# Optimization experiments

Hardware: AMD Instinct MI355X
Metric: run time of the kernel (lower is better)

## Reference

```python
import jax, jax.numpy as jnp
import numpy as np

KN = 2048       # 12*N spatio-temporal tokens
B = 4           # batch
D_MODEL = 512
N_HEADS = 8
HEAD_DIM = D_MODEL // N_HEADS
FACTOR = 5
U_PART = min(FACTOR * int(np.ceil(np.log(KN))), KN)  # sample_k == n_top == 40


def setup_inputs() -> dict:
    rng = jax.random.key(0)
    ks = jax.random.split(rng, 12)
    d = D_MODEL
    wscale = 1.0 / np.sqrt(d)  # xavier-ish init scale
    return {
        "query": jax.random.normal(ks[0], (KN, B, d), jnp.float32),
        "key": jax.random.normal(ks[1], (KN, B, d), jnp.float32),
        "value": jax.random.normal(ks[2], (KN, B, d), jnp.float32),
        "index_sample": jax.random.randint(ks[3], (KN, U_PART), 0, KN),
        "Wq": jax.random.normal(ks[4], (d, d), jnp.float32) * wscale,
        "bq": jnp.zeros((d,), jnp.float32),
        "Wk": jax.random.normal(ks[5], (d, d), jnp.float32) * wscale,
        "bk": jnp.zeros((d,), jnp.float32),
        "Wv": jax.random.normal(ks[6], (d, d), jnp.float32) * wscale,
        "bv": jnp.zeros((d,), jnp.float32),
        "Wo": jax.random.normal(ks[7], (d, d), jnp.float32) * wscale,
        "bo": jnp.zeros((d,), jnp.float32),
    }


def reference(query, key, value, index_sample, Wq, bq, Wk, bk, Wv, bv, Wo, bo):
    kN, Bb, d = query.shape
    H, E = N_HEADS, HEAD_DIM
    scaling = E ** -0.5

    # projections (torch Linear: x @ W.T + b); q is scaled before reshaping
    q = (query @ Wq.T + bq) * scaling
    k = key @ Wk.T + bk
    v = value @ Wv.T + bv

    # [kN, B, d] -> [B, H, kN, E]
    def to_bhne(x):
        return x.reshape(kN, Bb, H, E).transpose(1, 2, 0, 3)

    Q, K, V = to_bhne(q), to_bhne(k), to_bhne(v)

    # ProbSparse: sample U_PART keys per query row (shared index table)
    K_samp = K[:, :, index_sample, :]                       # [B,H,kN,S,E]
    QK_samp = jnp.einsum('bhne,bhnse->bhns', Q, K_samp)      # [B,H,kN,S]
    # sparsity measure M = max - mean(over full kN, as in source)
    M = QK_samp.max(axis=-1) - QK_samp.sum(axis=-1) / kN     # [B,H,kN]
    _, M_top = jax.lax.top_k(M, U_PART)                      # [B,H,S]

    # reduced queries attend over ALL keys
    Q_red = jnp.take_along_axis(Q, M_top[..., None], axis=2)  # [B,H,S,E]
    scores = jnp.einsum('bhse,bhne->bhsn', Q_red, K)          # [B,H,S,kN]
    attn = jax.nn.softmax(scores, axis=-1)
    upd = jnp.einsum('bhsn,bhne->bhse', attn, V)              # [B,H,S,E]

    # initial context = mean(V) broadcast; scatter-update the top rows
    ctx = jnp.broadcast_to(V.mean(axis=2, keepdims=True), V.shape)  # [B,H,kN,E]
    bi = jnp.arange(Bb)[:, None, None]
    hi = jnp.arange(H)[None, :, None]
    ctx = ctx.at[bi, hi, M_top].set(upd)

    out = ctx.transpose(0, 2, 1, 3).reshape(Bb, kN, d) @ Wo.T + bo  # [B,kN,d]
    return out
```

## Files before the change

### kernel.cpp

```cpp
#include <hip/hip_runtime.h>
#include <hip/hip_bf16.h>

#define KN 2048
#define BB 4
#define DM 512
#define NH 8
#define HE 64
#define UP 40
#define NBH 32
#define NROWS 8192
#define MiB(x) ((size_t)(x) << 20)

typedef __attribute__((ext_vector_type(8))) short short8;
typedef __attribute__((ext_vector_type(4))) float f32x4;

__device__ __forceinline__ ushort f2bf(float x) {
  unsigned u = __float_as_uint(x);
  unsigned r = (u + 0x7FFFu + ((u >> 16) & 1u)) >> 16;
  return (ushort)r;
}
__device__ __forceinline__ float bf2f(ushort h) {
  return __uint_as_float((unsigned)h << 16);
}

__global__ __launch_bounds__(256) void wsplit3_kernel(
    const float* __restrict__ W0, const float* __restrict__ W1,
    const float* __restrict__ W2, ushort* __restrict__ Wh,
    ushort* __restrict__ Wl) {
  const int which = blockIdx.x >> 9;
  const float* W = (which == 0) ? W0 : (which == 1) ? W1 : W2;
  size_t base = (size_t)which * 262144;
  int i = ((blockIdx.x & 511) * 256 + threadIdx.x) * 2;
  float2 v = *(const float2*)(W + i);
  ushort h0 = f2bf(v.x), h1 = f2bf(v.y);
  ushort l0 = f2bf(v.x - bf2f(h0)), l1 = f2bf(v.y - bf2f(h1));
  *(ushort2*)(Wh + base + i) = make_ushort2(h0, h1);
  *(ushort2*)(Wl + base + i) = make_ushort2(l0, l1);
}

#define APAD 40
__global__ __launch_bounds__(256) void gemm3_mfma(
    const float* __restrict__ A0, const float* __restrict__ A1,
    const float* __restrict__ A2,
    const ushort* __restrict__ Wh3, const ushort* __restrict__ Wl3,
    const float* __restrict__ bq, const float* __restrict__ bk,
    const float* __restrict__ bv, float* __restrict__ QKV) {
  __shared__ ushort AsH[2][64 * APAD];
  __shared__ ushort AsL[2][64 * APAD];

  const int which = blockIdx.x >> 8;
  const int local = blockIdx.x & 255;
  const int xcd = local & 7;
  const int idx = local >> 3;
  const int ot = idx >> 4;
  const int mt = xcd * 16 + (idx & 15);
  const int m0 = mt * 64, o0 = ot * 256;

  const float* A = (which == 0) ? A0 : (which == 1) ? A1 : A2;
  const ushort* Wh = Wh3 + (size_t)which * 262144;
  const ushort* Wl = Wl3 + (size_t)which * 262144;
  const float* bias = (which == 0) ? bq : (which == 1) ? bk : bv;
  float* C = QKV + (size_t)which * 8192 * 512;
  const float scale = (which == 0) ? 0.125f : 1.0f;

  const int tid = threadIdx.x;
  const int w = tid >> 6, lane = tid & 63;
  const int fr = lane & 15;
  const int kc = lane >> 4;

  f32x4 acc[4][4];
#pragma unroll
  for (int i = 0; i < 4; ++i)
#pragma unroll
    for (int j = 0; j < 4; ++j)
#pragma unroll
      for (int r = 0; r < 4; ++r) acc[i][j][r] = 0.f;

  const int srow0 = tid >> 3, sq0 = tid & 7;
  const int srow1 = (tid + 256) >> 3, sq1 = (tid + 256) & 7;

#define STAGE_A(BUF, K0)                                                    \
  do {                                                                      \
    float4 v0 = *(const float4*)(A + (size_t)(m0 + srow0) * 512 + (K0) + sq0 * 4); \
    float4 v1 = *(const float4*)(A + (size_t)(m0 + srow1) * 512 + (K0) + sq1 * 4); \
    ushort h0 = f2bf(v0.x), h1 = f2bf(v0.y), h2 = f2bf(v0.z), h3 = f2bf(v0.w); \
    *(ushort4*)(&AsH[BUF][srow0 * APAD + sq0 * 4]) = make_ushort4(h0, h1, h2, h3); \
    *(ushort4*)(&AsL[BUF][srow0 * APAD + sq0 * 4]) = make_ushort4(           \
        f2bf(v0.x - bf2f(h0)), f2bf(v0.y - bf2f(h1)),                        \
        f2bf(v0.z - bf2f(h2)), f2bf(v0.w - bf2f(h3)));                       \
    ushort g0 = f2bf(v1.x), g1 = f2bf(v1.y), g2 = f2bf(v1.z), g3 = f2bf(v1.w); \
    *(ushort4*)(&AsH[BUF][srow1 * APAD + sq1 * 4]) = make_ushort4(g0, g1, g2, g3); \
    *(ushort4*)(&AsL[BUF][srow1 * APAD + sq1 * 4]) = make_ushort4(           \
        f2bf(v1.x - bf2f(g0)), f2bf(v1.y - bf2f(g1)),                        \
        f2bf(v1.z - bf2f(g2)), f2bf(v1.w - bf2f(g3)));                       \
  } while (0)

  STAGE_A(0, 0);

#pragma unroll
  for (int it = 0; it < 16; ++it) {
    const int cur = it & 1;
    const int k0 = it * 32;
    __syncthreads();
    if (it + 1 < 16) STAGE_A(!cur ? 1 : 0, k0 + 32);

    short8 ah[4], al[4], bh[4], bl[4];
#pragma unroll
    for (int i = 0; i < 4; ++i) {
      int off = (i * 16 + fr) * APAD + kc * 8;
      ah[i] = *(const short8*)(&AsH[cur][off]);
      al[i] = *(const short8*)(&AsL[cur][off]);
    }
#pragma unroll
    for (int j = 0; j < 4; ++j) {
      size_t off = (size_t)(o0 + w * 64 + j * 16 + fr) * 512 + k0 + kc * 8;
      bh[j] = *(const short8*)(Wh + off);
      bl[j] = *(const short8*)(Wl + off);
    }
#pragma unroll
    for (int i = 0; i < 4; ++i)
#pragma unroll
      for (int j = 0; j < 4; ++j) {
        acc[i][j] = __builtin_amdgcn_mfma_f32_16x16x32_bf16(
            ah[i], bh[j], acc[i][j], 0, 0, 0);
        acc[i][j] = __builtin_amdgcn_mfma_f32_16x16x32_bf16(
            ah[i], bl[j], acc[i][j], 0, 0, 0);
        acc[i][j] = __builtin_amdgcn_mfma_f32_16x16x32_bf16(
            al[i], bh[j], acc[i][j], 0, 0, 0);
      }
  }

#pragma unroll
  for (int i = 0; i < 4; ++i)
#pragma unroll
    for (int j = 0; j < 4; ++j)
#pragma unroll
      for (int r = 0; r < 4; ++r) {
        int m = m0 + i * 16 + (lane >> 4) * 4 + r;
        int o = o0 + w * 64 + j * 16 + fr;
        C[(size_t)m * 512 + o] = (acc[i][j][r] + bias[o]) * scale;
      }
}

__global__ __launch_bounds__(256) void transposeK_kernel(
    const float* __restrict__ K, float* __restrict__ Kt) {
  const int bh = blockIdx.x & 31;
  const int nt = blockIdx.x >> 5;
  const int b = bh >> 3, h = bh & 7;
  const int n0 = nt * 128;
  const int tid = threadIdx.x;
  __shared__ float T[128][65];

#pragma unroll
  for (int i = 0; i < 8; ++i) {
    int flat = tid + i * 256;
    int r = flat >> 4;
    int c4 = flat & 15;
    float4 v = *(const float4*)(K + (((size_t)(n0 + r) * 4 + b) * 8 + h) * 64 + c4 * 4);
    T[r][c4 * 4 + 0] = v.x; T[r][c4 * 4 + 1] = v.y;
    T[r][c4 * 4 + 2] = v.z; T[r][c4 * 4 + 3] = v.w;
  }
  __syncthreads();

  const int nl = tid & 127;
  const int eg = tid >> 7;
#pragma unroll
  for (int e = eg * 32; e < eg * 32 + 32; ++e)
    Kt[((size_t)bh * 64 + e) * 2048 + n0 + nl] = T[nl][e];
}

__global__ __launch_bounds__(256) void mscore_kernel(
    const float* __restrict__ Q, const float* __restrict__ K,
    const int* __restrict__ idx, float* __restrict__ Mout) {
  const int bh = blockIdx.x & 31;
  const int c  = blockIdx.x >> 5;
  const int wv = threadIdx.x >> 6;
  const int lane = threadIdx.x & 63;
  const int n = c * 4 + wv;
  const int b = bh >> 3, h = bh & 7;
  const int g = lane >> 4;
  const int e16 = lane & 15;

  const float4 qv = *(const float4*)(Q + (((size_t)n * 4 + b) * 8 + h) * 64 + e16 * 4);

  float mx = -INFINITY, sm = 0.f;
#pragma unroll
  for (int it = 0; it < 10; ++it) {
    const int s = it * 4 + g;
    const int kn = idx[n * UP + s];
    const float4 kv = *(const float4*)(K + (((size_t)kn * 4 + b) * 8 + h) * 64 + e16 * 4);
    float d = qv.x * kv.x + qv.y * kv.y + qv.z * kv.z + qv.w * kv.w;
    d += __shfl_xor(d, 1);
    d += __shfl_xor(d, 2);
    d += __shfl_xor(d, 4);
    d += __shfl_xor(d, 8);
    mx = fmaxf(mx, d);
    sm += d;
  }
  mx = fmaxf(mx, __shfl_xor(mx, 16));
  mx = fmaxf(mx, __shfl_xor(mx, 32));
  sm += __shfl_xor(sm, 16);
  sm += __shfl_xor(sm, 32);
  if (lane == 0) Mout[(size_t)bh * 2048 + n] = mx - sm * (1.0f / (float)KN);
}

__global__ __launch_bounds__(256) void topk_kernel(
    const float* __restrict__ M, int* __restrict__ Mtop) {
  const int bh = blockIdx.x;
  __shared__ unsigned keys[2048];
  __shared__ int hist[256];
  __shared__ int suf[256];
  __shared__ int scal[2];
  __shared__ int ties[128];
  __shared__ int cnts[2];

  const int tid = threadIdx.x;
  const float* Mrow = M + (size_t)bh * 2048;
#pragma unroll
  for (int i = 0; i < 8; ++i) {
    int j = tid + i * 256;
    unsigned u = __float_as_uint(Mrow[j]);
    keys[j] = (u & 0x80000000u) ? ~u : (u | 0x80000000u);
  }
  if (tid < 2) cnts[tid] = 0;

  unsigned prefix = 0, prefmask = 0;
  int rank = UP;
#pragma unroll
  for (int shift = 24; shift >= 0; shift -= 8) {
    hist[tid] = 0;
    __syncthreads();
#pragma unroll
    for (int i = 0; i < 8; ++i) {
      unsigned k = keys[tid + i * 256];
      if ((k & prefmask) == prefix)
        atomicAdd(&hist[(k >> shift) & 0xFFu], 1);
    }
    __syncthreads();
    suf[tid] = hist[tid];
    __syncthreads();
#pragma unroll
    for (int off = 1; off < 256; off <<= 1) {
      int add = (tid + off < 256) ? suf[tid + off] : 0;
      __syncthreads();
      suf[tid] += add;
      __syncthreads();
    }
    {
      int above = suf[tid] - hist[tid];
      if (above < rank && rank <= suf[tid]) {
        scal[0] = tid;
        scal[1] = rank - above;
      }
    }
    __syncthreads();
    prefix |= ((unsigned)scal[0]) << shift;
    prefmask |= 0xFFu << shift;
    rank = scal[1];
    __syncthreads();
  }
  const unsigned T = prefix;

#pragma unroll
  for (int i = 0; i < 8; ++i) {
    int j = tid + i * 256;
    unsigned k = keys[j];
    if (k > T) {
      int p = atomicAdd(&cnts[0], 1);
      Mtop[bh * UP + p] = j;
    } else if (k == T) {
      int p = atomicAdd(&cnts[1], 1);
      if (p < 128) ties[p] = j;
    }
  }
  __syncthreads();
  if (tid == 0) {
    int base = cnts[0];
    int need = UP - base;
    int tc = cnts[1] < 128 ? cnts[1] : 128;
    for (int s = 0; s < need; ++s) {
      int best = 1 << 30, bj = 0;
      for (int j = 0; j < tc; ++j) {
        int v = ties[j];
        if (v < best) { best = v; bj = j; }
      }
      Mtop[bh * UP + base + s] = best;
      ties[bj] = 1 << 30;
    }
  }
}

__global__ __launch_bounds__(256) void meanv_part(
    const float* __restrict__ V, float* __restrict__ part) {
  const int rc = blockIdx.x >> 3;
  const int cc = blockIdx.x & 7;
  const int c = cc * 256 + threadIdx.x;
  const float* p = V + (size_t)rc * 64 * 2048 + c;
  float acc = 0.f;
#pragma unroll 8
  for (int i = 0; i < 64; ++i) acc += p[(size_t)i * 2048];
  part[(size_t)rc * 2048 + c] = acc;
}

__global__ __launch_bounds__(256) void meanv_final(
    const float* __restrict__ part, float* __restrict__ mnV) {
  const int c = blockIdx.x * 256 + threadIdx.x;
  float acc = 0.f;
#pragma unroll
  for (int r = 0; r < 32; ++r) acc += part[(size_t)r * 2048 + c];
  mnV[c] = acc * (1.0f / (float)KN);
}

__global__ __launch_bounds__(256) void meanout_kernel(
    const float* __restrict__ mnV, const float* __restrict__ Wo,
    const float* __restrict__ bo, float* __restrict__ mo) {
  const int b = blockIdx.x >> 3;
  const int oc = blockIdx.x & 7;
  const int ol = threadIdx.x & 63;
  const int kp = threadIdx.x >> 6;
  const int o = oc * 64 + ol;
  __shared__ float red[4][64];

  const float* m = mnV + b * 512;
  const float* w = Wo + (size_t)o * 512;
  float acc = 0.f;
#pragma unroll 8
  for (int k = kp * 128; k < kp * 128 + 128; ++k)
    acc = fmaf(m[k], w[k], acc);
  red[kp][ol] = acc;
  __syncthreads();
  if (threadIdx.x < 64) {
    float s = red[0][ol] + red[1][ol] + red[2][ol] + red[3][ol];
    mo[b * 512 + o] = s + bo[o];
  }
}

__global__ void fillout_kernel(const float* __restrict__ mo,
                               float* __restrict__ out) {
  size_t i = ((size_t)blockIdx.x * 256 + threadIdx.x) * 4;
  int d = (int)(i & 511);
  int b = (int)(i >> 20);
  float4 v = *(const float4*)(mo + (b << 9) + d);
  *(float4*)(out + i) = v;
}

__global__ __launch_bounds__(128) void fillsel_kernel(
    const int* __restrict__ Mtop, const float* __restrict__ mnV,
    float* __restrict__ ctx) {
  const int i = blockIdx.x;
  const int b = (i / UP) >> 3;
  const int row = b * 2048 + Mtop[i];
  float4 v = *(const float4*)(mnV + b * 512 + threadIdx.x * 4);
  *(float4*)(ctx + (size_t)row * 512 + threadIdx.x * 4) = v;
}

__global__ __launch_bounds__(256) void gemm_rows(
    const float* __restrict__ ctx, const float* __restrict__ W,
    const float* __restrict__ bias, const int* __restrict__ Mtop,
    float* __restrict__ out) {
  __shared__ float As[32][36];
  __shared__ float Ws[32][68];
  __shared__ int rsel[32];
  const int rt = blockIdx.x >> 3;
  const int ot = blockIdx.x & 7;
  const int o0 = ot * 64;
  const int tid = threadIdx.x;
  const int tx = tid & 15;
  const int ty = tid >> 4;

  if (tid < 32) {
    int g = rt * 32 + tid;
    int b = (g / UP) >> 3;
    rsel[tid] = b * 2048 + Mtop[g];
  }
  __syncthreads();

  float acc[2][4] = {};
  for (int k0 = 0; k0 < 512; k0 += 32) {
    {
      int row = tid >> 3, q = tid & 7;
      float4 av = *(const float4*)(ctx + (size_t)rsel[row] * 512 + k0 + q * 4);
      As[q * 4 + 0][row] = av.x; As[q * 4 + 1][row] = av.y;
      As[q * 4 + 2][row] = av.z; As[q * 4 + 3][row] = av.w;
    }
#pragma unroll
    for (int i = 0; i < 2; ++i) {
      int flat = tid + i * 256;
      int r = flat >> 3, q = flat & 7;
      float4 wv = *(const float4*)(W + (size_t)(o0 + r) * 512 + k0 + q * 4);
      Ws[q * 4 + 0][r] = wv.x; Ws[q * 4 + 1][r] = wv.y;
      Ws[q * 4 + 2][r] = wv.z; Ws[q * 4 + 3][r] = wv.w;
    }
    __syncthreads();
#pragma unroll
    for (int kk = 0; kk < 32; ++kk) {
      float a_[2], w_[4];
#pragma unroll
      for (int i = 0; i < 2; ++i) a_[i] = As[kk][ty * 2 + i];
#pragma unroll
      for (int j = 0; j < 4; ++j) w_[j] = Ws[kk][tx * 4 + j];
#pragma unroll
      for (int i = 0; i < 2; ++i)
#pragma unroll
        for (int j = 0; j < 4; ++j)
          acc[i][j] = fmaf(a_[i], w_[j], acc[i][j]);
    }
    __syncthreads();
  }

#pragma unroll
  for (int i = 0; i < 2; ++i) {
    int m = rsel[ty * 2 + i];
#pragma unroll
    for (int j = 0; j < 4; ++j) {
      int o = o0 + tx * 4 + j;
      out[(size_t)m * 512 + o] = acc[i][j] + bias[o];
    }
  }
}

#define QG 5
#define NC 4
__global__ __launch_bounds__(256) void attn_part(
    const float* __restrict__ Q, const float* __restrict__ Kt,
    const float* __restrict__ V, const int* __restrict__ Mtop,
    float* __restrict__ pmax, float* __restrict__ psum,
    float* __restrict__ pvp) {
  const int bh = blockIdx.x & 31;
  const int t  = blockIdx.x >> 5;
  const int g  = t & 7;
  const int ch = t >> 3;
  const int b = bh >> 3, h = bh & 7;
  const int tid = threadIdx.x;
  const int wv = tid >> 6, lane = tid & 63;
  const int n0 = ch * 512;

  __shared__ float qs[QG][64];
  __shared__ float p[QG][512];
  __shared__ float redm[QG][4];
  __shared__ float reds[QG][4];
  __shared__ float pvs[4][QG][64];

  for (int i = tid; i < QG * 64; i += 256) {
    int q = i >> 6, e = i & 63;
    int nq = Mtop[bh * UP + g * QG + q];
    qs[q][e] = Q[(((size_t)nq * 4 + b) * 8 + h) * 64 + e];
  }
  __syncthreads();

  const float* ktb = Kt + (size_t)bh * 64 * 2048;
  float d0[QG] = {}, d1[QG] = {};
  const int nb = n0 + tid * 2;
  for (int e = 0; e < 64; ++e) {
    float2 kv = *(const float2*)(ktb + (size_t)e * 2048 + nb);
#pragma unroll
    for (int q = 0; q < QG; ++q) {
      float qe = qs[q][e];
      d0[q] = fmaf(qe, kv.x, d0[q]);
      d1[q] = fmaf(qe, kv.y, d1[q]);
    }
  }

#pragma unroll
  for (int q = 0; q < QG; ++q) {
    float m_ = fmaxf(d0[q], d1[q]);
#pragma unroll
    for (int off = 1; off < 64; off <<= 1)
      m_ = fmaxf(m_, __shfl_xor(m_, off));
    if (lane == 0) redm[q][wv] = m_;
  }
  __syncthreads();
  float gm[QG];
#pragma unroll
  for (int q = 0; q < QG; ++q)
    gm[q] = fmaxf(fmaxf(redm[q][0], redm[q][1]),
                  fmaxf(redm[q][2], redm[q][3]));

  float ls[QG];
#pragma unroll
  for (int q = 0; q < QG; ++q) {
    float e0 = __expf(d0[q] - gm[q]);
    float e1 = __expf(d1[q] - gm[q]);
    p[q][tid * 2] = e0;
    p[q][tid * 2 + 1] = e1;
    ls[q] = e0 + e1;
  }
#pragma unroll
  for (int q = 0; q < QG; ++q) {
    float s_ = ls[q];
#pragma unroll
    for (int off = 1; off < 64; off <<= 1)
      s_ += __shfl_xor(s_, off);
    if (lane == 0) reds[q][wv] = s_;
  }
  __syncthreads();
  float den[QG];
#pragma unroll
  for (int q = 0; q < QG; ++q)
    den[q] = reds[q][0] + reds[q][1] + reds[q][2] + reds[q][3];

  float acc[QG] = {};
  for (int nn = wv * 128; nn < wv * 128 + 128; ++nn) {
    float v = V[(((size_t)(n0 + nn) * 4 + b) * 8 + h) * 64 + lane];
#pragma unroll
    for (int q = 0; q < QG; ++q) acc[q] = fmaf(p[q][nn], v, acc[q]);
  }
#pragma unroll
  for (int q = 0; q < QG; ++q) pvs[wv][q][lane] = acc[q];
  __syncthreads();

  for (int i = tid; i < QG * 64; i += 256) {
    int q = i >> 6, e = i & 63;
    int slot = bh * UP + g * QG + q;
    float pv = pvs[0][q][e] + pvs[1][q][e] + pvs[2][q][e] + pvs[3][q][e];
    pvp[((size_t)slot * NC + ch) * 64 + e] = pv;
    if (e == 0) {
      pmax[slot * NC + ch] = gm[q];
      psum[slot * NC + ch] = den[q];
    }
  }
}

__global__ __launch_bounds__(64) void attn_combine(
    const float* __restrict__ pmax, const float* __restrict__ psum,
    const float* __restrict__ pvp, float* __restrict__ upd) {
  const int slot = blockIdx.x;
  const int e = threadIdx.x;
  float m = -INFINITY;
#pragma unroll
  for (int ch = 0; ch < NC; ++ch) m = fmaxf(m, pmax[slot * NC + ch]);
  float den = 0.f, num = 0.f;
#pragma unroll
  for (int ch = 0; ch < NC; ++ch) {
    float w = __expf(pmax[slot * NC + ch] - m);
    den = fmaf(w, psum[slot * NC + ch], den);
    num = fmaf(w, pvp[((size_t)slot * NC + ch) * 64 + e], num);
  }
  upd[(size_t)slot * 64 + e] = num / den;
}

__global__ void scatter_kernel(const float* __restrict__ upd,
                               const int* __restrict__ Mtop,
                               float* __restrict__ ctx) {
  const int blk = blockIdx.x;
  const int bh = blk / UP;
  const int b = bh >> 3, h = bh & 7;
  const int n = Mtop[blk];
  ctx[((size_t)(b * 2048 + n)) * 512 + h * 64 + threadIdx.x] =
      upd[(size_t)blk * 64 + threadIdx.x];
}

extern "C" void kernel_launch(void* const* d_in, const int* in_sizes, int n_in,
                              void* d_out, int out_size, void* d_ws,
                              size_t ws_size, hipStream_t stream) {
  const float* query = (const float*)d_in[0];
  const float* key   = (const float*)d_in[1];
  const float* value = (const float*)d_in[2];
  const int*   idxs  = (const int*)d_in[3];
  const float* Wq = (const float*)d_in[4];
  const float* bq = (const float*)d_in[5];
  const float* Wk = (const float*)d_in[6];
  const float* bk = (const float*)d_in[7];
  const float* Wv = (const float*)d_in[8];
  const float* bv = (const float*)d_in[9];
  const float* Wo = (const float*)d_in[10];
  const float* bo = (const float*)d_in[11];
  float* out = (float*)d_out;

  char* ws = (char*)d_ws;
  float*  Mbuf  = (float*)(ws + 0);
  float*  upd   = (float*)(ws + 262144);
  float*  mnV   = (float*)(ws + 589824);
  int*    Mtop  = (int*)  (ws + 598016);
  float*  vpart = (float*)(ws + 634880);
  float*  mo    = (float*)(ws + 941312);
  float*  QKV   = (float*)(ws + MiB(1));
  float*  Q     = QKV;
  float*  K     = (float*)(ws + MiB(17));
  float*  V     = (float*)(ws + MiB(33));
  float*  Kt    = (float*)(ws + MiB(49));
  ushort* Wh3   = (ushort*)(ws + MiB(65));
  ushort* Wl3   = (ushort*)(ws + MiB(65) + 1572864);
  float*  pmax  = (float*)(ws + MiB(68));
  float*  psum  = (float*)(ws + MiB(68) + 32768);
  float*  pvp   = (float*)(ws + MiB(68) + 65536);
  float*  ctx   = Q;

  wsplit3_kernel<<<1536, 256, 0, stream>>>(Wq, Wk, Wv, Wh3, Wl3);
  gemm3_mfma<<<768, 256, 0, stream>>>(query, key, value, Wh3, Wl3,
                                      bq, bk, bv, QKV);

  transposeK_kernel<<<512, 256, 0, stream>>>(K, Kt);

  mscore_kernel<<<16384, 256, 0, stream>>>(Q, K, idxs, Mbuf);
  topk_kernel<<<NBH, 256, 0, stream>>>(Mbuf, Mtop);

  meanv_part<<<256, 256, 0, stream>>>(V, vpart);
  meanv_final<<<8, 256, 0, stream>>>(vpart, mnV);

  attn_part<<<NBH * 32, 256, 0, stream>>>(Q, Kt, V, Mtop, pmax, psum, pvp);
  attn_combine<<<NBH * UP, 64, 0, stream>>>(pmax, psum, pvp, upd);

  fillsel_kernel<<<NBH * UP, 128, 0, stream>>>(Mtop, mnV, ctx);
  scatter_kernel<<<NBH * UP, 64, 0, stream>>>(upd, Mtop, ctx);

  meanout_kernel<<<32, 256, 0, stream>>>(mnV, Wo, bo, mo);
  fillout_kernel<<<4096, 256, 0, stream>>>(mo, out);
  gemm_rows<<<320, 256, 0, stream>>>(ctx, Wo, bo, Mtop, out);
}
```

Before: 188.2 us.

## Merge independent stages into multi-role kernels to cut launch count

Independent kernels are packed into shared launches that pick their role from the block index. The K transpose, M-score and V partial sum become one kernel; top-k and the V-mean finish become another; attention partials run alongside the mean-output GEMV; the two fill kernels are merged; and combine is fused with scatter, which removes the upd buffer. The goal is fewer launches and less idle time between small kernels. The cost is heterogeneous blocks with a larger shared-memory footprint per block, which may lower occupancy for the lighter roles.

```diff
diff --git a/kernel.cpp b/kernel.cpp
--- a/kernel.cpp
+++ b/kernel.cpp
@@ -142,79 +142,107 @@
       }
 }
 
-__global__ __launch_bounds__(256) void transposeK_kernel(
-    const float* __restrict__ K, float* __restrict__ Kt) {
-  const int bh = blockIdx.x & 31;
-  const int nt = blockIdx.x >> 5;
-  const int b = bh >> 3, h = bh & 7;
-  const int n0 = nt * 128;
+__global__ __launch_bounds__(256) void prep3_kernel(
+    const float* __restrict__ K, float* __restrict__ Kt,
+    const float* __restrict__ Q, const int* __restrict__ idx,
+    float* __restrict__ Mout, const float* __restrict__ V,
+    float* __restrict__ vpart) {
+  __shared__ float T[64][65];
+  const int bid = blockIdx.x;
   const int tid = threadIdx.x;
-  __shared__ float T[128][65];
-
-#pragma unroll
-  for (int i = 0; i < 8; ++i) {
-    int flat = tid + i * 256;
-    int r = flat >> 4;
-    int c4 = flat & 15;
-    float4 v = *(const float4*)(K + (((size_t)(n0 + r) * 4 + b) * 8 + h) * 64 + c4 * 4);
-    T[r][c4 * 4 + 0] = v.x; T[r][c4 * 4 + 1] = v.y;
-    T[r][c4 * 4 + 2] = v.z; T[r][c4 * 4 + 3] = v.w;
-  }
-  __syncthreads();
-
-  const int nl = tid & 127;
-  const int eg = tid >> 7;
-#pragma unroll
-  for (int e = eg * 32; e < eg * 32 + 32; ++e)
-    Kt[((size_t)bh * 64 + e) * 2048 + n0 + nl] = T[nl][e];
-}
-
-__global__ __launch_bounds__(256) void mscore_kernel(
-    const float* __restrict__ Q, const float* __restrict__ K,
-    const int* __restrict__ idx, float* __restrict__ Mout) {
-  const int bh = blockIdx.x & 31;
-  const int c  = blockIdx.x >> 5;
-  const int wv = threadIdx.x >> 6;
-  const int lane = threadIdx.x & 63;
-  const int n = c * 4 + wv;
-  const int b = bh >> 3, h = bh & 7;
-  const int g = lane >> 4;
-  const int e16 = lane & 15;
-
-  const float4 qv = *(const float4*)(Q + (((size_t)n * 4 + b) * 8 + h) * 64 + e16 * 4);
-
-  float mx = -INFINITY, sm = 0.f;
-#pragma unroll
-  for (int it = 0; it < 10; ++it) {
-    const int s = it * 4 + g;
-    const int kn = idx[n * UP + s];
-    const float4 kv = *(const float4*)(K + (((size_t)kn * 4 + b) * 8 + h) * 64 + e16 * 4);
-    float d = qv.x * kv.x + qv.y * kv.y + qv.z * kv.z + qv.w * kv.w;
-    d += __shfl_xor(d, 1);
-    d += __shfl_xor(d, 2);
-    d += __shfl_xor(d, 4);
-    d += __shfl_xor(d, 8);
-    mx = fmaxf(mx, d);
-    sm += d;
-  }
-  mx = fmaxf(mx, __shfl_xor(mx, 16));
-  mx = fmaxf(mx, __shfl_xor(mx, 32));
-  sm += __shfl_xor(sm, 16);
-  sm += __shfl_xor(sm, 32);
-  if (lane == 0) Mout[(size_t)bh * 2048 + n] = mx - sm * (1.0f / (float)KN);
-}
-
-__global__ __launch_bounds__(256) void topk_kernel(
-    const float* __restrict__ M, int* __restrict__ Mtop) {
-  const int bh = blockIdx.x;
+
+  if (bid < 1024) {
+    const int bh = bid & 31;
+    const int nt = bid >> 5;
+    const int b = bh >> 3, h = bh & 7;
+    const int n0 = nt * 64;
+#pragma unroll
+    for (int i = 0; i < 4; ++i) {
+      int flat = tid + i * 256;
+      int r = flat >> 4;
+      int c4 = flat & 15;
+      float4 v = *(const float4*)(K + (((size_t)(n0 + r) * 4 + b) * 8 + h) * 64 + c4 * 4);
+      T[r][c4 * 4 + 0] = v.x; T[r][c4 * 4 + 1] = v.y;
+      T[r][c4 * 4 + 2] = v.z; T[r][c4 * 4 + 3] = v.w;
+    }
+    __syncthreads();
+    const int nl = tid & 63;
+    const int eg = tid >> 6;
+#pragma unroll
+    for (int e = eg * 16; e < eg * 16 + 16; ++e)
+      Kt[((size_t)bh * 64 + e) * 2048 + n0 + nl] = T[nl][e];
+    return;
+  }
+
+  if (bid < 1024 + 16384) {
+    const int vb = bid - 1024;
+    const int bh = vb & 31;
+    const int c  = vb >> 5;
+    const int wv = tid >> 6;
+    const int lane = tid & 63;
+    const int n = c * 4 + wv;
+    const int b = bh >> 3, h = bh & 7;
+    const int g = lane >> 4;
+    const int e16 = lane & 15;
+
+    const float4 qv = *(const float4*)(Q + (((size_t)n * 4 + b) * 8 + h) * 64 + e16 * 4);
+
+    float mx = -INFINITY, sm = 0.f;
+#pragma unroll
+    for (int it = 0; it < 10; ++it) {
+      const int s = it * 4 + g;
+      const int kn = idx[n * UP + s];
+      const float4 kv = *(const float4*)(K + (((size_t)kn * 4 + b) * 8 + h) * 64 + e16 * 4);
+      float d = qv.x * kv.x + qv.y * kv.y + qv.z * kv.z + qv.w * kv.w;
+      d += __shfl_xor(d, 1);
+      d += __shfl_xor(d, 2);
+      d += __shfl_xor(d, 4);
+      d += __shfl_xor(d, 8);
+      mx = fmaxf(mx, d);
+      sm += d;
+    }
+    mx = fmaxf(mx, __shfl_xor(mx, 16));
+    mx = fmaxf(mx, __shfl_xor(mx, 32));
+    sm += __shfl_xor(sm, 16);
+    sm += __shfl_xor(sm, 32);
+    if (lane == 0) Mout[(size_t)bh * 2048 + n] = mx - sm * (1.0f / (float)KN);
+    return;
+  }
+
+  {
+    const int vb = bid - 17408;
+    const int rc = vb >> 3;
+    const int cc = vb & 7;
+    const int c = cc * 256 + tid;
+    const float* p = V + (size_t)rc * 64 * 2048 + c;
+    float acc = 0.f;
+#pragma unroll 8
+    for (int i = 0; i < 64; ++i) acc += p[(size_t)i * 2048];
+    vpart[(size_t)rc * 2048 + c] = acc;
+  }
+}
+
+__global__ __launch_bounds__(256) void sel2_kernel(
+    const float* __restrict__ M, int* __restrict__ Mtop,
+    const float* __restrict__ part, float* __restrict__ mnV) {
   __shared__ unsigned keys[2048];
   __shared__ int hist[256];
   __shared__ int suf[256];
   __shared__ int scal[2];
   __shared__ int ties[128];
   __shared__ int cnts[2];
-
   const int tid = threadIdx.x;
+
+  if (blockIdx.x >= 32) {
+    const int c = (blockIdx.x - 32) * 256 + tid;
+    float acc = 0.f;
+#pragma unroll
+    for (int r = 0; r < 32; ++r) acc += part[(size_t)r * 2048 + c];
+    mnV[c] = acc * (1.0f / (float)KN);
+    return;
+  }
+
+  const int bh = blockIdx.x;
   const float* Mrow = M + (size_t)bh * 2048;
 #pragma unroll
   for (int i = 0; i < 8; ++i) {
@@ -290,68 +318,176 @@
   }
 }
 
-__global__ __launch_bounds__(256) void meanv_part(
-    const float* __restrict__ V, float* __restrict__ part) {
-  const int rc = blockIdx.x >> 3;
-  const int cc = blockIdx.x & 7;
-  const int c = cc * 256 + threadIdx.x;
-  const float* p = V + (size_t)rc * 64 * 2048 + c;
-  float acc = 0.f;
+#define QG 5
+#define NC 4
+__global__ __launch_bounds__(256) void attnmean_kernel(
+    const float* __restrict__ Q, const float* __restrict__ Kt,
+    const float* __restrict__ V, const int* __restrict__ Mtop,
+    float* __restrict__ pmax, float* __restrict__ psum,
+    float* __restrict__ pvp, const float* __restrict__ mnV,
+    const float* __restrict__ Wo, const float* __restrict__ bo,
+    float* __restrict__ mo) {
+  __shared__ float qs[QG][64];
+  __shared__ float p[QG][512];
+  __shared__ float redm[QG][4];
+  __shared__ float reds[QG][4];
+  __shared__ float pvs[4][QG][64];
+  const int tid = threadIdx.x;
+
+  if (blockIdx.x >= 1024) {
+    const int mb = blockIdx.x - 1024;
+    const int b = mb >> 3;
+    const int oc = mb & 7;
+    const int ol = tid & 63;
+    const int kp = tid >> 6;
+    const int o = oc * 64 + ol;
+    const float* m = mnV + b * 512;
+    const float* w = Wo + (size_t)o * 512;
+    float acc = 0.f;
 #pragma unroll 8
-  for (int i = 0; i < 64; ++i) acc += p[(size_t)i * 2048];
-  part[(size_t)rc * 2048 + c] = acc;
-}
-
-__global__ __launch_bounds__(256) void meanv_final(
-    const float* __restrict__ part, float* __restrict__ mnV) {
-  const int c = blockIdx.x * 256 + threadIdx.x;
-  float acc = 0.f;
-#pragma unroll
-  for (int r = 0; r < 32; ++r) acc += part[(size_t)r * 2048 + c];
-  mnV[c] = acc * (1.0f / (float)KN);
-}
-
-__global__ __launch_bounds__(256) void meanout_kernel(
-    const float* __restrict__ mnV, const float* __restrict__ Wo,
-    const float* __restrict__ bo, float* __restrict__ mo) {
-  const int b = blockIdx.x >> 3;
-  const int oc = blockIdx.x & 7;
-  const int ol = threadIdx.x & 63;
-  const int kp = threadIdx.x >> 6;
-  const int o = oc * 64 + ol;
-  __shared__ float red[4][64];
-
-  const float* m = mnV + b * 512;
-  const float* w = Wo + (size_t)o * 512;
-  float acc = 0.f;
-#pragma unroll 8
-  for (int k = kp * 128; k < kp * 128 + 128; ++k)
-    acc = fmaf(m[k], w[k], acc);
-  red[kp][ol] = acc;
+    for (int k = kp * 128; k < kp * 128 + 128; ++k)
+      acc = fmaf(m[k], w[k], acc);
+    redm[0][0] = redm[0][0];
+    __shared__ float red[4][64];
+    red[kp][ol] = acc;
+    __syncthreads();
+    if (tid < 64) {
+      float s = red[0][ol] + red[1][ol] + red[2][ol] + red[3][ol];
+      mo[b * 512 + o] = s + bo[o];
+    }
+    return;
+  }
+
+  const int bh = blockIdx.x & 31;
+  const int t  = blockIdx.x >> 5;
+  const int g  = t & 7;
+  const int ch = t >> 3;
+  const int b = bh >> 3, h = bh & 7;
+  const int wv = tid >> 6, lane = tid & 63;
+  const int n0 = ch * 512;
+
+  for (int i = tid; i < QG * 64; i += 256) {
+    int q = i >> 6, e = i & 63;
+    int nq = Mtop[bh * UP + g * QG + q];
+    qs[q][e] = Q[(((size_t)nq * 4 + b) * 8 + h) * 64 + e];
+  }
   __syncthreads();
-  if (threadIdx.x < 64) {
-    float s = red[0][ol] + red[1][ol] + red[2][ol] + red[3][ol];
-    mo[b * 512 + o] = s + bo[o];
-  }
-}
-
-__global__ void fillout_kernel(const float* __restrict__ mo,
-                               float* __restrict__ out) {
-  size_t i = ((size_t)blockIdx.x * 256 + threadIdx.x) * 4;
+
+  const float* ktb = Kt + (size_t)bh * 64 * 2048;
+  float d0[QG] = {}, d1[QG] = {};
+  const int nb = n0 + tid * 2;
+  for (int e = 0; e < 64; ++e) {
+    float2 kv = *(const float2*)(ktb + (size_t)e * 2048 + nb);
+#pragma unroll
+    for (int q = 0; q < QG; ++q) {
+      float qe = qs[q][e];
+      d0[q] = fmaf(qe, kv.x, d0[q]);
+      d1[q] = fmaf(qe, kv.y, d1[q]);
+    }
+  }
+
+#pragma unroll
+  for (int q = 0; q < QG; ++q) {
+    float m_ = fmaxf(d0[q], d1[q]);
+#pragma unroll
+    for (int off = 1; off < 64; off <<= 1)
+      m_ = fmaxf(m_, __shfl_xor(m_, off));
+    if (lane == 0) redm[q][wv] = m_;
+  }
+  __syncthreads();
+  float gm[QG];
+#pragma unroll
+  for (int q = 0; q < QG; ++q)
+    gm[q] = fmaxf(fmaxf(redm[q][0], redm[q][1]),
+                  fmaxf(redm[q][2], redm[q][3]));
+
+  float ls[QG];
+#pragma unroll
+  for (int q = 0; q < QG; ++q) {
+    float e0 = __expf(d0[q] - gm[q]);
+    float e1 = __expf(d1[q] - gm[q]);
+    p[q][tid * 2] = e0;
+    p[q][tid * 2 + 1] = e1;
+    ls[q] = e0 + e1;
+  }
+#pragma unroll
+  for (int q = 0; q < QG; ++q) {
+    float s_ = ls[q];
+#pragma unroll
+    for (int off = 1; off < 64; off <<= 1)
+      s_ += __shfl_xor(s_, off);
+    if (lane == 0) reds[q][wv] = s_;
+  }
+  __syncthreads();
+  float den[QG];
+#pragma unroll
+  for (int q = 0; q < QG; ++q)
+    den[q] = reds[q][0] + reds[q][1] + reds[q][2] + reds[q][3];
+
+  float acc[QG] = {};
+  for (int nn = wv * 128; nn < wv * 128 + 128; ++nn) {
+    float v = V[(((size_t)(n0 + nn) * 4 + b) * 8 + h) * 64 + lane];
+#pragma unroll
+    for (int q = 0; q < QG; ++q) acc[q] = fmaf(p[q][nn], v, acc[q]);
+  }
+#pragma unroll
+  for (int q = 0; q < QG; ++q) pvs[wv][q][lane] = acc[q];
+  __syncthreads();
+
+  for (int i = tid; i < QG * 64; i += 256) {
+    int q = i >> 6, e = i & 63;
+    int slot = bh * UP + g * QG + q;
+    float pv = pvs[0][q][e] + pvs[1][q][e] + pvs[2][q][e] + pvs[3][q][e];
+    pvp[((size_t)slot * NC + ch) * 64 + e] = pv;
+    if (e == 0) {
+      pmax[slot * NC + ch] = gm[q];
+      psum[slot * NC + ch] = den[q];
+    }
+  }
+}
+
+__global__ __launch_bounds__(256) void fill2_kernel(
+    const int* __restrict__ Mtop, const float* __restrict__ mnV,
+    float* __restrict__ ctx, const float* __restrict__ mo,
+    float* __restrict__ out) {
+  const int tid = threadIdx.x;
+  if (blockIdx.x < 1280) {
+    if (tid < 128) {
+      const int i = blockIdx.x;
+      const int b = (i / UP) >> 3;
+      const int row = b * 2048 + Mtop[i];
+      float4 v = *(const float4*)(mnV + b * 512 + tid * 4);
+      *(float4*)(ctx + (size_t)row * 512 + tid * 4) = v;
+    }
+    return;
+  }
+  size_t i = ((size_t)(blockIdx.x - 1280) * 256 + tid) * 4;
   int d = (int)(i & 511);
   int b = (int)(i >> 20);
   float4 v = *(const float4*)(mo + (b << 9) + d);
   *(float4*)(out + i) = v;
 }
 
-__global__ __launch_bounds__(128) void fillsel_kernel(
-    const int* __restrict__ Mtop, const float* __restrict__ mnV,
+__global__ __launch_bounds__(64) void combine_scatter_kernel(
+    const float* __restrict__ pmax, const float* __restrict__ psum,
+    const float* __restrict__ pvp, const int* __restrict__ Mtop,
     float* __restrict__ ctx) {
-  const int i = blockIdx.x;
-  const int b = (i / UP) >> 3;
-  const int row = b * 2048 + Mtop[i];
-  float4 v = *(const float4*)(mnV + b * 512 + threadIdx.x * 4);
-  *(float4*)(ctx + (size_t)row * 512 + threadIdx.x * 4) = v;
+  const int slot = blockIdx.x;
+  const int e = threadIdx.x;
+  const int bh = slot / UP;
+  const int b = bh >> 3, h = bh & 7;
+  const int n = Mtop[slot];
+  float m = -INFINITY;
+#pragma unroll
+  for (int ch = 0; ch < NC; ++ch) m = fmaxf(m, pmax[slot * NC + ch]);
+  float den = 0.f, num = 0.f;
+#pragma unroll
+  for (int ch = 0; ch < NC; ++ch) {
+    float w = __expf(pmax[slot * NC + ch] - m);
+    den = fmaf(w, psum[slot * NC + ch], den);
+    num = fmaf(w, pvp[((size_t)slot * NC + ch) * 64 + e], num);
+  }
+  ctx[((size_t)(b * 2048 + n)) * 512 + h * 64 + e] = num / den;
 }
 
 __global__ __launch_bounds__(256) void gemm_rows(
@@ -417,137 +553,6 @@
       out[(size_t)m * 512 + o] = acc[i][j] + bias[o];
     }
   }
-}
-
-#define QG 5
-#define NC 4
-__global__ __launch_bounds__(256) void attn_part(
-    const float* __restrict__ Q, const float* __restrict__ Kt,
-    const float* __restrict__ V, const int* __restrict__ Mtop,
-    float* __restrict__ pmax, float* __restrict__ psum,
-    float* __restrict__ pvp) {
-  const int bh = blockIdx.x & 31;
-  const int t  = blockIdx.x >> 5;
-  const int g  = t & 7;
-  const int ch = t >> 3;
-  const int b = bh >> 3, h = bh & 7;
-  const int tid = threadIdx.x;
-  const int wv = tid >> 6, lane = tid & 63;
-  const int n0 = ch * 512;
-
-  __shared__ float qs[QG][64];
-  __shared__ float p[QG][512];
-  __shared__ float redm[QG][4];
-  __shared__ float reds[QG][4];
-  __shared__ float pvs[4][QG][64];
-
-  for (int i = tid; i < QG * 64; i += 256) {
-    int q = i >> 6, e = i & 63;
-    int nq = Mtop[bh * UP + g * QG + q];
-    qs[q][e] = Q[(((size_t)nq * 4 + b) * 8 + h) * 64 + e];
-  }
-  __syncthreads();
-
-  const float* ktb = Kt + (size_t)bh * 64 * 2048;
-  float d0[QG] = {}, d1[QG] = {};
-  const int nb = n0 + tid * 2;
-  for (int e = 0; e < 64; ++e) {
-    float2 kv = *(const float2*)(ktb + (size_t)e * 2048 + nb);
-#pragma unroll
-    for (int q = 0; q < QG; ++q) {
-      float qe = qs[q][e];
-      d0[q] = fmaf(qe, kv.x, d0[q]);
-      d1[q] = fmaf(qe, kv.y, d1[q]);
-    }
-  }
-
-#pragma unroll
-  for (int q = 0; q < QG; ++q) {
-    float m_ = fmaxf(d0[q], d1[q]);
-#pragma unroll
-    for (int off = 1; off < 64; off <<= 1)
-      m_ = fmaxf(m_, __shfl_xor(m_, off));
-    if (lane == 0) redm[q][wv] = m_;
-  }
-  __syncthreads();
-  float gm[QG];
-#pragma unroll
-  for (int q = 0; q < QG; ++q)
-    gm[q] = fmaxf(fmaxf(redm[q][0], redm[q][1]),
-                  fmaxf(redm[q][2], redm[q][3]));
-
-  float ls[QG];
-#pragma unroll
-  for (int q = 0; q < QG; ++q) {
-    float e0 = __expf(d0[q] - gm[q]);
-    float e1 = __expf(d1[q] - gm[q]);
-    p[q][tid * 2] = e0;
-    p[q][tid * 2 + 1] = e1;
-    ls[q] = e0 + e1;
-  }
-#pragma unroll
-  for (int q = 0; q < QG; ++q) {
-    float s_ = ls[q];
-#pragma unroll
-    for (int off = 1; off < 64; off <<= 1)
-      s_ += __shfl_xor(s_, off);
-    if (lane == 0) reds[q][wv] = s_;
-  }
-  __syncthreads();
-  float den[QG];
-#pragma unroll
-  for (int q = 0; q < QG; ++q)
-    den[q] = reds[q][0] + reds[q][1] + reds[q][2] + reds[q][3];
-
-  float acc[QG] = {};
-  for (int nn = wv * 128; nn < wv * 128 + 128; ++nn) {
-    float v = V[(((size_t)(n0 + nn) * 4 + b) * 8 + h) * 64 + lane];
-#pragma unroll
-    for (int q = 0; q < QG; ++q) acc[q] = fmaf(p[q][nn], v, acc[q]);
-  }
-#pragma unroll
-  for (int q = 0; q < QG; ++q) pvs[wv][q][lane] = acc[q];
-  __syncthreads();
-
-  for (int i = tid; i < QG * 64; i += 256) {
-    int q = i >> 6, e = i & 63;
-    int slot = bh * UP + g * QG + q;
-    float pv = pvs[0][q][e] + pvs[1][q][e] + pvs[2][q][e] + pvs[3][q][e];
-    pvp[((size_t)slot * NC + ch) * 64 + e] = pv;
-    if (e == 0) {
-      pmax[slot * NC + ch] = gm[q];
-      psum[slot * NC + ch] = den[q];
-    }
-  }
-}
-
-__global__ __launch_bounds__(64) void attn_combine(
-    const float* __restrict__ pmax, const float* __restrict__ psum,
-    const float* __restrict__ pvp, float* __restrict__ upd) {
-  const int slot = blockIdx.x;
-  const int e = threadIdx.x;
-  float m = -INFINITY;
-#pragma unroll
-  for (int ch = 0; ch < NC; ++ch) m = fmaxf(m, pmax[slot * NC + ch]);
-  float den = 0.f, num = 0.f;
-#pragma unroll
-  for (int ch = 0; ch < NC; ++ch) {
-    float w = __expf(pmax[slot * NC + ch] - m);
-    den = fmaf(w, psum[slot * NC + ch], den);
-    num = fmaf(w, pvp[((size_t)slot * NC + ch) * 64 + e], num);
-  }
-  upd[(size_t)slot * 64 + e] = num / den;
-}
-
-__global__ void scatter_kernel(const float* __restrict__ upd,
-                               const int* __restrict__ Mtop,
-                               float* __restrict__ ctx) {
-  const int blk = blockIdx.x;
-  const int bh = blk / UP;
-  const int b = bh >> 3, h = bh & 7;
-  const int n = Mtop[blk];
-  ctx[((size_t)(b * 2048 + n)) * 512 + h * 64 + threadIdx.x] =
-      upd[(size_t)blk * 64 + threadIdx.x];
 }
 
 extern "C" void kernel_launch(void* const* d_in, const int* in_sizes, int n_in,
@@ -569,7 +574,6 @@
 
   char* ws = (char*)d_ws;
   float*  Mbuf  = (float*)(ws + 0);
-  float*  upd   = (float*)(ws + 262144);
   float*  mnV   = (float*)(ws + 589824);
   int*    Mtop  = (int*)  (ws + 598016);
   float*  vpart = (float*)(ws + 634880);
@@ -590,21 +594,13 @@
   gemm3_mfma<<<768, 256, 0, stream>>>(query, key, value, Wh3, Wl3,
                                       bq, bk, bv, QKV);
 
-  transposeK_kernel<<<512, 256, 0, stream>>>(K, Kt);
-
-  mscore_kernel<<<16384, 256, 0, stream>>>(Q, K, idxs, Mbuf);
-  topk_kernel<<<NBH, 256, 0, stream>>>(Mbuf, Mtop);
-
-  meanv_part<<<256, 256, 0, stream>>>(V, vpart);
-  meanv_final<<<8, 256, 0, stream>>>(vpart, mnV);
-
-  attn_part<<<NBH * 32, 256, 0, stream>>>(Q, Kt, V, Mtop, pmax, psum, pvp);
-  attn_combine<<<NBH * UP, 64, 0, stream>>>(pmax, psum, pvp, upd);
-
-  fillsel_kernel<<<NBH * UP, 128, 0, stream>>>(Mtop, mnV, ctx);
-  scatter_kernel<<<NBH * UP, 64, 0, stream>>>(upd, Mtop, ctx);
-
-  meanout_kernel<<<32, 256, 0, stream>>>(mnV, Wo, bo, mo);
-  fillout_kernel<<<4096, 256, 0, stream>>>(mo, out);
+  prep3_kernel<<<17664, 256, 0, stream>>>(K, Kt, Q, idxs, Mbuf, V, vpart);
+  sel2_kernel<<<40, 256, 0, stream>>>(Mbuf, Mtop, vpart, mnV);
+
+  attnmean_kernel<<<1056, 256, 0, stream>>>(Q, Kt, V, Mtop, pmax, psum, pvp,
+                                            mnV, Wo, bo, mo);
+  fill2_kernel<<<5376, 256, 0, stream>>>(Mtop, mnV, ctx, mo, out);
+  combine_scatter_kernel<<<NBH * UP, 64, 0, stream>>>(pmax, psum, pvp,
+                                                      Mtop, ctx);
   gemm_rows<<<320, 256, 0, stream>>>(ctx, Wo, bo, Mtop, out);
 }
```

Measured after the change: 170.8 us. -9.3%, faster.
